# Performance work log

Hardware: AMD Instinct MI355X
Metric: run time of the kernel (lower is better)

Reference implementation:

```python
import jax, jax.numpy as jnp
import numpy as np

E = 1_000_000
D = 64
N = 100_000


def setup_inputs() -> dict:
    key = jax.random.key(0)
    k1, k2 = jax.random.split(key)
    mj = jax.random.normal(k1, (E, D), dtype=jnp.float32)
    edge_index = jax.random.randint(k2, (2, E), 0, N, dtype=jnp.int64)
    return {"mj": mj, "edge_index": edge_index, "num_nodes": N}


def reference(mj, edge_index, num_nodes):
    # source_to_target=True: scatter-add edge features into target nodes (edge_index[1])
    # mj: [E, D], edge_index: [2, E] -> vi: [num_nodes, D]
    vi = jax.ops.segment_sum(mj, edge_index[1, :], num_segments=num_nodes)
    return vi
```

## Files before the change

kernel.cpp:

```cpp
#include <hip/hip_runtime.h>


#define FEAT 64
#define CAP 64

__global__ void __launch_bounds__(256)
scatter_kernel(const int* __restrict__ tgt, int* __restrict__ cursor,
               int* __restrict__ bucket, int E) {
    int i = blockIdx.x * 256 + threadIdx.x;
    if (i < E) {
        int t = tgt[i];
        int pos = atomicAdd(&cursor[t], 1);
        if (pos < CAP) bucket[t * CAP + pos] = i;
    }
}

__global__ void __launch_bounds__(256)
gather_kernel(const float4* __restrict__ mj4, const int* __restrict__ cursor,
              const int* __restrict__ bucket, float4* __restrict__ out4, int N) {
    int gid = (blockIdx.x * 256 + threadIdx.x) >> 4;
    int l = threadIdx.x & 15;
    if (gid >= N) return;
    int deg = cursor[gid];
    if (deg > CAP) deg = CAP;
    const int* row = bucket + gid * CAP;
    float4 acc = make_float4(0.f, 0.f, 0.f, 0.f);
    int j = 0;
    for (; j + 1 < deg; j += 2) {
        int e0 = row[j];
        int e1 = row[j + 1];
        float4 a = mj4[(size_t)e0 * 16 + l];
        float4 b = mj4[(size_t)e1 * 16 + l];
        acc.x += a.x + b.x;
        acc.y += a.y + b.y;
        acc.z += a.z + b.z;
        acc.w += a.w + b.w;
    }
    if (j < deg) {
        int e0 = row[j];
        float4 a = mj4[(size_t)e0 * 16 + l];
        acc.x += a.x;
        acc.y += a.y;
        acc.z += a.z;
        acc.w += a.w;
    }
    out4[(size_t)gid * 16 + l] = acc;
}

extern "C" void kernel_launch(void* const* d_in, const int* in_sizes, int n_in,
                              void* d_out, int out_size, void* d_ws, size_t ws_size,
                              hipStream_t stream) {
    const float* mj = (const float*)d_in[0];
    const int* edge_index = (const int*)d_in[1];
    int E = in_sizes[1] / 2;
    const int* tgt = edge_index + E;
    int N = out_size / FEAT;

    int* cursor = (int*)d_ws;
    int* bucket = cursor + N;

    hipMemsetAsync(cursor, 0, (size_t)N * sizeof(int), stream);

    int eblk = (E + 255) / 256;
    scatter_kernel<<<eblk, 256, 0, stream>>>(tgt, cursor, bucket, E);

    int gblk = (N * 16 + 255) / 256;
    gather_kernel<<<gblk, 256, 0, stream>>>(
        (const float4*)mj, cursor, bucket, (float4*)d_out, N);
}
```

Before: 123.2 us.

## Shrink per-node buckets and add overflow list with cleanup kernel

Halves the per-node bucket capacity and routes edges past capacity to a global overflow list, which a single-block cleanup kernel then adds into the output with atomics. The gather loop is unrolled to four edges, and it uses nontemporal loads for edge features and nontemporal stores for the output. The aim is to shrink the bucket footprint and reduce cache pollution from streaming data. The cost is an extra kernel launch and a serial cleanup that would be slow if many nodes exceeded the capacity.

```diff
diff --git a/kernel.cpp b/kernel.cpp
--- a/kernel.cpp
+++ b/kernel.cpp
@@ -1,50 +1,64 @@
 #include <hip/hip_runtime.h>
 
 
+typedef float f4 __attribute__((ext_vector_type(4)));
+
 #define FEAT 64
-#define CAP 64
+#define CAP 32
+#define OVF_CAP (1 << 20)
 
 __global__ void __launch_bounds__(256)
 scatter_kernel(const int* __restrict__ tgt, int* __restrict__ cursor,
-               int* __restrict__ bucket, int E) {
+               int* __restrict__ bucket, int* __restrict__ ovf_cnt,
+               int* __restrict__ ovf, int E) {
     int i = blockIdx.x * 256 + threadIdx.x;
-    if (i < E) {
-        int t = tgt[i];
-        int pos = atomicAdd(&cursor[t], 1);
-        if (pos < CAP) bucket[t * CAP + pos] = i;
+    if (i >= E) return;
+    int t = tgt[i];
+    int pos = atomicAdd(&cursor[t], 1);
+    if (pos < CAP) {
+        __builtin_nontemporal_store(i, &bucket[t * CAP + pos]);
+    } else {
+        int q = atomicAdd(ovf_cnt, 1);
+        if (q < OVF_CAP) { ovf[2 * q] = t; ovf[2 * q + 1] = i; }
     }
 }
 
 __global__ void __launch_bounds__(256)
-gather_kernel(const float4* __restrict__ mj4, const int* __restrict__ cursor,
-              const int* __restrict__ bucket, float4* __restrict__ out4, int N) {
+gather_kernel(const f4* __restrict__ mj4, const int* __restrict__ cursor,
+              const int* __restrict__ bucket, f4* __restrict__ out4, int N) {
     int gid = (blockIdx.x * 256 + threadIdx.x) >> 4;
     int l = threadIdx.x & 15;
     if (gid >= N) return;
     int deg = cursor[gid];
     if (deg > CAP) deg = CAP;
     const int* row = bucket + gid * CAP;
-    float4 acc = make_float4(0.f, 0.f, 0.f, 0.f);
+    f4 acc = {0.f, 0.f, 0.f, 0.f};
     int j = 0;
-    for (; j + 1 < deg; j += 2) {
-        int e0 = row[j];
-        int e1 = row[j + 1];
-        float4 a = mj4[(size_t)e0 * 16 + l];
-        float4 b = mj4[(size_t)e1 * 16 + l];
-        acc.x += a.x + b.x;
-        acc.y += a.y + b.y;
-        acc.z += a.z + b.z;
-        acc.w += a.w + b.w;
+    for (; j + 3 < deg; j += 4) {
+        int e0 = row[j], e1 = row[j + 1], e2 = row[j + 2], e3 = row[j + 3];
+        f4 a = __builtin_nontemporal_load(&mj4[(size_t)e0 * 16 + l]);
+        f4 b = __builtin_nontemporal_load(&mj4[(size_t)e1 * 16 + l]);
+        f4 c = __builtin_nontemporal_load(&mj4[(size_t)e2 * 16 + l]);
+        f4 d = __builtin_nontemporal_load(&mj4[(size_t)e3 * 16 + l]);
+        acc += a + b + c + d;
     }
-    if (j < deg) {
-        int e0 = row[j];
-        float4 a = mj4[(size_t)e0 * 16 + l];
-        acc.x += a.x;
-        acc.y += a.y;
-        acc.z += a.z;
-        acc.w += a.w;
+    for (; j < deg; ++j) {
+        acc += __builtin_nontemporal_load(&mj4[(size_t)row[j] * 16 + l]);
     }
-    out4[(size_t)gid * 16 + l] = acc;
+    __builtin_nontemporal_store(acc, &out4[(size_t)gid * 16 + l]);
+}
+
+__global__ void __launch_bounds__(256)
+cleanup_kernel(const float* __restrict__ mj, const int* __restrict__ ovf_cnt,
+               const int* __restrict__ ovf, float* __restrict__ out) {
+    int n = *ovf_cnt;
+    if (n > OVF_CAP) n = OVF_CAP;
+    int sub = threadIdx.x >> 6;
+    int lane = threadIdx.x & 63;
+    for (int k = sub; k < n; k += 4) {
+        int t = ovf[2 * k], e = ovf[2 * k + 1];
+        atomicAdd(&out[(size_t)t * FEAT + lane], mj[(size_t)e * FEAT + lane]);
+    }
 }
 
 extern "C" void kernel_launch(void* const* d_in, const int* in_sizes, int n_in,
@@ -56,15 +70,19 @@
     const int* tgt = edge_index + E;
     int N = out_size / FEAT;
 
-    int* cursor = (int*)d_ws;
-    int* bucket = cursor + N;
+    int* cursor  = (int*)d_ws;
+    int* ovf_cnt = cursor + N;
+    int* ovf     = ovf_cnt + 1;
+    int* bucket  = ovf + 2 * OVF_CAP;
 
-    hipMemsetAsync(cursor, 0, (size_t)N * sizeof(int), stream);
+    hipMemsetAsync(cursor, 0, (size_t)(N + 1) * sizeof(int), stream);
 
     int eblk = (E + 255) / 256;
-    scatter_kernel<<<eblk, 256, 0, stream>>>(tgt, cursor, bucket, E);
+    scatter_kernel<<<eblk, 256, 0, stream>>>(tgt, cursor, bucket, ovf_cnt, ovf, E);
 
     int gblk = (N * 16 + 255) / 256;
     gather_kernel<<<gblk, 256, 0, stream>>>(
-        (const float4*)mj, cursor, bucket, (float4*)d_out, N);
+        (const f4*)mj, cursor, bucket, (f4*)d_out, N);
+
+    cleanup_kernel<<<1, 256, 0, stream>>>(mj, ovf_cnt, ovf, (float*)d_out);
 }
```

After: 148.4 us. +20.4%, slower.
